# Optimization experiments

Hardware: AMD Instinct MI355X
Metric: run time of the kernel (lower is better)

Reference implementation:

```python
import jax, jax.numpy as jnp
import numpy as np

B, D, NF, L, G = 8192, 4096, 16, 32, 64  # batch, input_dim, num_factors, latent_per_factor, num groups
K = D // G  # group size (contiguous equal-size partition of columns)


def setup_inputs() -> dict:
    key = jax.random.key(0)
    k0, k1, k2, k3 = jax.random.split(key, 4)
    x = jax.random.normal(k0, (B, D), dtype=jnp.float32)
    # encoder: Linear(D,128) -> ReLU -> Linear(128, NF*L)
    W1 = jax.random.normal(k1, (D, 128), dtype=jnp.float32) * 0.02
    b1 = jnp.zeros((128,), dtype=jnp.float32)
    W2 = jax.random.normal(k2, (128, NF * L), dtype=jnp.float32) * 0.02
    b2 = jnp.zeros((NF * L,), dtype=jnp.float32)
    # k_matrix decoders: one [K, L] matrix per group, stacked -> [G, K, L]
    decoders = jax.random.normal(k3, (G, K, L), dtype=jnp.float32)
    return {"x": x, "W1": W1, "b1": b1, "W2": W2, "b2": b2, "decoders": decoders}


def reference(x, W1, b1, W2, b2, decoders):
    # encoder
    z = jax.nn.relu(x @ W1 + b1) @ W2 + b2                 # [B, NF*L]
    # reconstructions[:, group_g] = sum_j z_j @ D_g^T  ==  (sum_j z_j) @ D_g^T
    z_sum = z.reshape(x.shape[0], NF, L).sum(axis=1)        # [B, L]
    recon = jnp.einsum('bl,gkl->bgk', z_sum, decoders)      # [B, G, K]
    recon = recon.reshape(x.shape[0], G * K)                # [B, D] (contiguous groups)
    return (z, recon)
```

## Files before the change

kernel.cpp:

```cpp
#include <hip/hip_runtime.h>
#include <hip/hip_bf16.h>

#define BATCH 8192
#define DIN   4096
#define H1    128
#define NLAT  512
#define LAT   32
#define BM    32
#define BK    128
#define NSTEP (DIN / BK)
#define APITCH 136

typedef short bf16x8 __attribute__((ext_vector_type(8)));
typedef float f32x4  __attribute__((ext_vector_type(4)));

static __device__ __forceinline__ unsigned short f2bf(float f) {
  union { float f; unsigned u; } v; v.f = f;
  return (unsigned short)((v.u + 0x7FFFu + ((v.u >> 16) & 1u)) >> 16);
}

__global__ void prep_all(const float* __restrict__ W1, const float* __restrict__ W2,
                         const float* __restrict__ dec,
                         unsigned short* __restrict__ W1B,
                         unsigned short* __restrict__ W2B,
                         float* __restrict__ decT) {
  int b = blockIdx.x;
  int t = threadIdx.x;
  if (b < 256) {
    int gi = (b << 2) + (t >> 6);
    int lane = t & 63;
    int kb = ((gi >> 3) << 5) + ((lane >> 4) << 3);
    int c = ((gi & 7) << 4) + (lane & 15);
    union { bf16x8 v; unsigned short u[8]; } o;
#pragma unroll
    for (int j = 0; j < 8; j++) o.u[j] = f2bf(W1[(size_t)(kb + j) * H1 + c]);
    *(bf16x8*)(W1B + (((size_t)gi << 6) + lane) * 8) = o.v;
  } else if (b < 288) {
    int gi = ((b - 256) << 2) + (t >> 6);
    int lane = t & 63;
    int kb = ((gi >> 5) << 5) + ((lane >> 4) << 3);
    int c = ((gi & 31) << 4) + (lane & 15);
    union { bf16x8 v; unsigned short u[8]; } o;
#pragma unroll
    for (int j = 0; j < 8; j++) o.u[j] = f2bf(W2[(size_t)(kb + j) * NLAT + c]);
    *(bf16x8*)(W2B + (((size_t)gi << 6) + lane) * 8) = o.v;
  } else {
    __shared__ float tbuf[32][33];
    int d0 = (b - 288) * 32;
    int tx = t & 31, ty = t >> 5;
#pragma unroll
    for (int i = 0; i < 32; i += 8)
      tbuf[ty + i][tx] = dec[(size_t)(d0 + ty + i) * LAT + tx];
    __syncthreads();
#pragma unroll
    for (int i = 0; i < 32; i += 8)
      decT[(size_t)(ty + i) * DIN + (d0 + tx)] = tbuf[tx][ty + i];
  }
}

__global__ __launch_bounds__(512, 2) void enc_kernel(
    const float* __restrict__ x, const unsigned short* __restrict__ W1B,
    const unsigned short* __restrict__ W2B,
    const float* __restrict__ b1, const float* __restrict__ b2,
    float* __restrict__ zout, float* __restrict__ zsumg) {
  __shared__ unsigned short As[2][BM * APITCH];
  __shared__ unsigned short hs[BM * APITCH];
  __shared__ float zsp[8][32][32];

  const int t = threadIdx.x;
  const int rbase = blockIdx.x << 5;
  const int w = t >> 6, lane = t & 63;
  const int g = lane >> 4, fr = lane & 15;

  const int srow = t >> 4, skq = (t & 15) << 3;
  const float* xp = x + (size_t)(rbase + srow) * DIN + skq;
  const int wofs = srow * APITCH + skq;

  f32x4 acc[2];
  acc[0] = (f32x4){0.f, 0.f, 0.f, 0.f};
  acc[1] = (f32x4){0.f, 0.f, 0.f, 0.f};

  {
    f32x4 ra0 = *(const f32x4*)xp;
    f32x4 ra1 = *(const f32x4*)(xp + 4);
    union { bf16x8 v; unsigned short u[8]; } o;
#pragma unroll
    for (int j = 0; j < 4; j++) { o.u[j] = f2bf(ra0[j]); o.u[4 + j] = f2bf(ra1[j]); }
    *(bf16x8*)(&As[0][wofs]) = o.v;
  }
  __syncthreads();

  for (int s = 0; s < NSTEP; ++s) {
    f32x4 ra0, ra1;
    const bool more = (s + 1) < NSTEP;
    if (more) {
      ra0 = *(const f32x4*)(xp + (s + 1) * BK);
      ra1 = *(const f32x4*)(xp + (s + 1) * BK + 4);
    }
    const unsigned short* ab = &As[s & 1][0];
#pragma unroll
    for (int k32 = 0; k32 < 4; ++k32) {
      bf16x8 bv = *(const bf16x8*)(W1B + (((size_t)(((s << 2) + k32) << 3) + w) << 9) + (lane << 3));
      bf16x8 a0 = *(const bf16x8*)(ab + fr * APITCH + (((k32 << 2) + g) << 3));
      bf16x8 a1 = *(const bf16x8*)(ab + (16 + fr) * APITCH + (((k32 << 2) + g) << 3));
      acc[0] = __builtin_amdgcn_mfma_f32_16x16x32_bf16(a0, bv, acc[0], 0, 0, 0);
      acc[1] = __builtin_amdgcn_mfma_f32_16x16x32_bf16(a1, bv, acc[1], 0, 0, 0);
    }
    if (more) {
      union { bf16x8 v; unsigned short u[8]; } o;
#pragma unroll
      for (int j = 0; j < 4; j++) { o.u[j] = f2bf(ra0[j]); o.u[4 + j] = f2bf(ra1[j]); }
      *(bf16x8*)(&As[(s + 1) & 1][wofs]) = o.v;
    }
    __syncthreads();
  }

  {
    const int col = (w << 4) + fr;
    const float b1v = b1[col];
#pragma unroll
    for (int rg = 0; rg < 2; rg++)
#pragma unroll
      for (int j = 0; j < 4; j++) {
        float h = fmaxf(acc[rg][j] + b1v, 0.f);
        hs[((rg << 4) + (g << 2) + j) * APITCH + col] = f2bf(h);
      }
  }
  __syncthreads();

  f32x4 acc2[2][4];
#pragma unroll
  for (int i = 0; i < 2; i++)
#pragma unroll
    for (int j = 0; j < 4; j++) acc2[i][j] = (f32x4){0.f, 0.f, 0.f, 0.f};
#pragma unroll
  for (int k32 = 0; k32 < 4; ++k32) {
    bf16x8 a0 = *(const bf16x8*)(hs + fr * APITCH + (((k32 << 2) + g) << 3));
    bf16x8 a1 = *(const bf16x8*)(hs + (16 + fr) * APITCH + (((k32 << 2) + g) << 3));
#pragma unroll
    for (int cfl = 0; cfl < 4; ++cfl) {
      bf16x8 bv = *(const bf16x8*)(W2B + (((size_t)((k32 << 5) + (w << 2) + cfl)) << 9) + (lane << 3));
      acc2[0][cfl] = __builtin_amdgcn_mfma_f32_16x16x32_bf16(a0, bv, acc2[0][cfl], 0, 0, 0);
      acc2[1][cfl] = __builtin_amdgcn_mfma_f32_16x16x32_bf16(a1, bv, acc2[1][cfl], 0, 0, 0);
    }
  }

  {
    float b2v[4];
#pragma unroll
    for (int cfl = 0; cfl < 4; ++cfl) b2v[cfl] = b2[(w << 6) + (cfl << 4) + fr];
#pragma unroll
    for (int rg = 0; rg < 2; rg++) {
      f32x4 zv[4];
#pragma unroll
      for (int cfl = 0; cfl < 4; ++cfl) {
#pragma unroll
        for (int j = 0; j < 4; j++) zv[cfl][j] = acc2[rg][cfl][j] + b2v[cfl];
        const int row = rbase + (rg << 4) + (g << 2);
        const int col = (w << 6) + (cfl << 4) + fr;
#pragma unroll
        for (int j = 0; j < 4; j++)
          zout[(size_t)(row + j) * NLAT + col] = zv[cfl][j];
      }
#pragma unroll
      for (int j = 0; j < 4; j++) {
        const int row = (rg << 4) + (g << 2) + j;
        zsp[w][row][fr]      = zv[0][j] + zv[2][j];
        zsp[w][row][16 + fr] = zv[1][j] + zv[3][j];
      }
    }
  }
  __syncthreads();
#pragma unroll
  for (int i = 0; i < 2; i++) {
    int idx = t + (i << 9);
    int r = idx >> 5, l = idx & 31;
    float s = 0.f;
#pragma unroll
    for (int w8 = 0; w8 < 8; w8++) s += zsp[w8][r][l];
    zsumg[(size_t)(rbase + r) * LAT + l] = s;
  }
}

__global__ __launch_bounds__(256) void recon_kernel(
    const float* __restrict__ zsumg, const float* __restrict__ decT,
    float* __restrict__ rout) {
  __shared__ float zs[32][32];
  int t = threadIdx.x;
  int rbase = (blockIdx.x >> 4) << 5;
  int dcol0 = (blockIdx.x & 15) << 8;
  {
    int r = t >> 3, c4 = (t & 7) << 2;
    *(f32x4*)&zs[r][c4] = *(const f32x4*)(zsumg + (size_t)(rbase + r) * LAT + c4);
  }
  __syncthreads();
  int wq = t >> 6, lane = t & 63;
  int r0 = wq << 3;
  int dcol = dcol0 + (lane << 2);
  f32x4 acc[8];
#pragma unroll
  for (int r = 0; r < 8; r++) acc[r] = (f32x4){0.f, 0.f, 0.f, 0.f};
#pragma unroll 8
  for (int l = 0; l < 32; l++) {
    f32x4 dv = *(const f32x4*)(decT + (size_t)l * DIN + dcol);
#pragma unroll
    for (int r = 0; r < 8; r++) {
      float zv = zs[r0 + r][l];
#pragma unroll
      for (int j = 0; j < 4; j++) acc[r][j] += zv * dv[j];
    }
  }
#pragma unroll
  for (int r = 0; r < 8; r++)
    *(f32x4*)(rout + (size_t)(rbase + r0 + r) * DIN + dcol) = acc[r];
}

extern "C" void kernel_launch(void* const* d_in, const int* in_sizes, int n_in,
                              void* d_out, int out_size, void* d_ws, size_t ws_size,
                              hipStream_t stream) {
  const float* x   = (const float*)d_in[0];
  const float* W1  = (const float*)d_in[1];
  const float* b1  = (const float*)d_in[2];
  const float* W2  = (const float*)d_in[3];
  const float* b2  = (const float*)d_in[4];
  const float* dec = (const float*)d_in[5];
  float* zout = (float*)d_out;
  float* rout = zout + (size_t)BATCH * NLAT;

  char* ws = (char*)d_ws;
  unsigned short* W1B = (unsigned short*)ws;
  unsigned short* W2B = (unsigned short*)(ws + (1u << 20));
  float* decT  = (float*)(ws + (1u << 20) + (1u << 17));
  float* zsumg = (float*)(ws + (1u << 20) + (1u << 17) + (1u << 19));

  prep_all<<<dim3(416), 256, 0, stream>>>(W1, W2, dec, W1B, W2B, decT);
  enc_kernel<<<dim3(BATCH / BM), 512, 0, stream>>>(x, W1B, W2B, b1, b2, zout, zsumg);
  recon_kernel<<<dim3(4096), 256, 0, stream>>>(zsumg, decT, rout);
}
```

Measured before the change: 91.06 us.

## Fuse reconstruction into encoder kernel with smaller row tiles and deeper prefetch

Merges the encoder and reconstruction kernels into a single kernel. Each block now computes z for 16 rows, reduces z_sum in shared memory, then writes the 16x4096 reconstruction directly, which removes the zsumg round trip and one launch. The row tile drops from 32 to 16 so there are twice as many blocks, and x loads are prefetched four steps ahead. In exchange, W1 B-fragments are reused across half as many rows, and each block's tail now streams a large output with only 16 accumulators per thread, which may lengthen per-block time and add register pressure.

```diff
diff --git a/kernel.cpp b/kernel.cpp
--- a/kernel.cpp
+++ b/kernel.cpp
@@ -6,17 +6,25 @@
 #define H1    128
 #define NLAT  512
 #define LAT   32
-#define BM    32
+#define BM    16
 #define BK    128
 #define NSTEP (DIN / BK)
 #define APITCH 136
 
 typedef short bf16x8 __attribute__((ext_vector_type(8)));
+typedef short bf16x4 __attribute__((ext_vector_type(4)));
 typedef float f32x4  __attribute__((ext_vector_type(4)));
 
 static __device__ __forceinline__ unsigned short f2bf(float f) {
   union { float f; unsigned u; } v; v.f = f;
   return (unsigned short)((v.u + 0x7FFFu + ((v.u >> 16) & 1u)) >> 16);
+}
+
+static __device__ __forceinline__ void cvtw4(unsigned short* p, f32x4 v) {
+  union { bf16x4 v; unsigned short u[4]; } o;
+#pragma unroll
+  for (int j = 0; j < 4; j++) o.u[j] = f2bf(v[j]);
+  *(bf16x4*)p = o.v;
 }
 
 __global__ void prep_all(const float* __restrict__ W1, const float* __restrict__ W2,
@@ -58,161 +66,132 @@
   }
 }
 
-__global__ __launch_bounds__(512, 2) void enc_kernel(
+__global__ __launch_bounds__(512, 2) void fused_kernel(
     const float* __restrict__ x, const unsigned short* __restrict__ W1B,
     const unsigned short* __restrict__ W2B,
     const float* __restrict__ b1, const float* __restrict__ b2,
-    float* __restrict__ zout, float* __restrict__ zsumg) {
+    const float* __restrict__ decT,
+    float* __restrict__ zout, float* __restrict__ rout) {
   __shared__ unsigned short As[2][BM * APITCH];
   __shared__ unsigned short hs[BM * APITCH];
-  __shared__ float zsp[8][32][32];
+  __shared__ float zsp[8][BM][32];
+  __shared__ float zs[BM][32];
 
   const int t = threadIdx.x;
-  const int rbase = blockIdx.x << 5;
+  const int rbase = blockIdx.x << 4;
   const int w = t >> 6, lane = t & 63;
   const int g = lane >> 4, fr = lane & 15;
 
-  const int srow = t >> 4, skq = (t & 15) << 3;
+  const int srow = t >> 5, skq = (t & 31) << 2;
   const float* xp = x + (size_t)(rbase + srow) * DIN + skq;
   const int wofs = srow * APITCH + skq;
 
-  f32x4 acc[2];
-  acc[0] = (f32x4){0.f, 0.f, 0.f, 0.f};
-  acc[1] = (f32x4){0.f, 0.f, 0.f, 0.f};
-
-  {
-    f32x4 ra0 = *(const f32x4*)xp;
-    f32x4 ra1 = *(const f32x4*)(xp + 4);
-    union { bf16x8 v; unsigned short u[8]; } o;
-#pragma unroll
-    for (int j = 0; j < 4; j++) { o.u[j] = f2bf(ra0[j]); o.u[4 + j] = f2bf(ra1[j]); }
-    *(bf16x8*)(&As[0][wofs]) = o.v;
-  }
-  __syncthreads();
-
-  for (int s = 0; s < NSTEP; ++s) {
-    f32x4 ra0, ra1;
-    const bool more = (s + 1) < NSTEP;
-    if (more) {
-      ra0 = *(const f32x4*)(xp + (s + 1) * BK);
-      ra1 = *(const f32x4*)(xp + (s + 1) * BK + 4);
-    }
-    const unsigned short* ab = &As[s & 1][0];
-#pragma unroll
-    for (int k32 = 0; k32 < 4; ++k32) {
-      bf16x8 bv = *(const bf16x8*)(W1B + (((size_t)(((s << 2) + k32) << 3) + w) << 9) + (lane << 3));
-      bf16x8 a0 = *(const bf16x8*)(ab + fr * APITCH + (((k32 << 2) + g) << 3));
-      bf16x8 a1 = *(const bf16x8*)(ab + (16 + fr) * APITCH + (((k32 << 2) + g) << 3));
-      acc[0] = __builtin_amdgcn_mfma_f32_16x16x32_bf16(a0, bv, acc[0], 0, 0, 0);
-      acc[1] = __builtin_amdgcn_mfma_f32_16x16x32_bf16(a1, bv, acc[1], 0, 0, 0);
-    }
-    if (more) {
-      union { bf16x8 v; unsigned short u[8]; } o;
-#pragma unroll
-      for (int j = 0; j < 4; j++) { o.u[j] = f2bf(ra0[j]); o.u[4 + j] = f2bf(ra1[j]); }
-      *(bf16x8*)(&As[(s + 1) & 1][wofs]) = o.v;
-    }
-    __syncthreads();
-  }
+  f32x4 acc = (f32x4){0.f, 0.f, 0.f, 0.f};
+
+  cvtw4(&As[0][wofs], *(const f32x4*)xp);
+  f32x4 pf1 = *(const f32x4*)(xp + 1 * BK);
+  f32x4 pf2 = *(const f32x4*)(xp + 2 * BK);
+  f32x4 pf3 = *(const f32x4*)(xp + 3 * BK);
+  f32x4 pf0 = *(const f32x4*)(xp + 4 * BK);
+  __syncthreads();
+
+#define ASTEP(S, PF) do {                                                    \
+    const unsigned short* ab = &As[(S) & 1][0];                              \
+    _Pragma("unroll")                                                        \
+    for (int k32 = 0; k32 < 4; ++k32) {                                      \
+      bf16x8 bv = *(const bf16x8*)(W1B +                                     \
+          ((((size_t)(((S) << 2) + k32) << 3) + w) << 9) + (lane << 3));     \
+      bf16x8 a0 = *(const bf16x8*)(ab + fr * APITCH + (((k32 << 2) + g) << 3)); \
+      acc = __builtin_amdgcn_mfma_f32_16x16x32_bf16(a0, bv, acc, 0, 0, 0);   \
+    }                                                                        \
+    if ((S) + 1 < NSTEP) {                                                   \
+      cvtw4(&As[((S) + 1) & 1][wofs], PF);                                   \
+      if ((S) + 5 < NSTEP) PF = *(const f32x4*)(xp + ((S) + 5) * BK);        \
+    }                                                                        \
+    __syncthreads();                                                         \
+  } while (0)
+
+  for (int s = 0; s < NSTEP; s += 4) {
+    ASTEP(s, pf1);
+    ASTEP(s + 1, pf2);
+    ASTEP(s + 2, pf3);
+    ASTEP(s + 3, pf0);
+  }
+#undef ASTEP
 
   {
     const int col = (w << 4) + fr;
     const float b1v = b1[col];
 #pragma unroll
-    for (int rg = 0; rg < 2; rg++)
-#pragma unroll
-      for (int j = 0; j < 4; j++) {
-        float h = fmaxf(acc[rg][j] + b1v, 0.f);
-        hs[((rg << 4) + (g << 2) + j) * APITCH + col] = f2bf(h);
-      }
-  }
-  __syncthreads();
-
-  f32x4 acc2[2][4];
-#pragma unroll
-  for (int i = 0; i < 2; i++)
-#pragma unroll
-    for (int j = 0; j < 4; j++) acc2[i][j] = (f32x4){0.f, 0.f, 0.f, 0.f};
+    for (int j = 0; j < 4; j++) {
+      float h = fmaxf(acc[j] + b1v, 0.f);
+      hs[((g << 2) + j) * APITCH + col] = f2bf(h);
+    }
+  }
+  __syncthreads();
+
+  f32x4 acc2[4];
+#pragma unroll
+  for (int i = 0; i < 4; i++) acc2[i] = (f32x4){0.f, 0.f, 0.f, 0.f};
 #pragma unroll
   for (int k32 = 0; k32 < 4; ++k32) {
     bf16x8 a0 = *(const bf16x8*)(hs + fr * APITCH + (((k32 << 2) + g) << 3));
-    bf16x8 a1 = *(const bf16x8*)(hs + (16 + fr) * APITCH + (((k32 << 2) + g) << 3));
 #pragma unroll
     for (int cfl = 0; cfl < 4; ++cfl) {
-      bf16x8 bv = *(const bf16x8*)(W2B + (((size_t)((k32 << 5) + (w << 2) + cfl)) << 9) + (lane << 3));
-      acc2[0][cfl] = __builtin_amdgcn_mfma_f32_16x16x32_bf16(a0, bv, acc2[0][cfl], 0, 0, 0);
-      acc2[1][cfl] = __builtin_amdgcn_mfma_f32_16x16x32_bf16(a1, bv, acc2[1][cfl], 0, 0, 0);
-    }
-  }
-
+      bf16x8 bv = *(const bf16x8*)(W2B +
+          (((size_t)((k32 << 5) + (w << 2) + cfl)) << 9) + (lane << 3));
+      acc2[cfl] = __builtin_amdgcn_mfma_f32_16x16x32_bf16(a0, bv, acc2[cfl], 0, 0, 0);
+    }
+  }
   {
-    float b2v[4];
-#pragma unroll
-    for (int cfl = 0; cfl < 4; ++cfl) b2v[cfl] = b2[(w << 6) + (cfl << 4) + fr];
-#pragma unroll
-    for (int rg = 0; rg < 2; rg++) {
-      f32x4 zv[4];
-#pragma unroll
-      for (int cfl = 0; cfl < 4; ++cfl) {
-#pragma unroll
-        for (int j = 0; j < 4; j++) zv[cfl][j] = acc2[rg][cfl][j] + b2v[cfl];
-        const int row = rbase + (rg << 4) + (g << 2);
-        const int col = (w << 6) + (cfl << 4) + fr;
-#pragma unroll
-        for (int j = 0; j < 4; j++)
-          zout[(size_t)(row + j) * NLAT + col] = zv[cfl][j];
+    f32x4 zv[4];
+#pragma unroll
+    for (int cfl = 0; cfl < 4; ++cfl) {
+      const float b2v = b2[(w << 6) + (cfl << 4) + fr];
+#pragma unroll
+      for (int j = 0; j < 4; j++) zv[cfl][j] = acc2[cfl][j] + b2v;
+    }
+    const int row0 = g << 2;
+#pragma unroll
+    for (int j = 0; j < 4; j++) {
+#pragma unroll
+      for (int cfl = 0; cfl < 4; ++cfl)
+        zout[(size_t)(rbase + row0 + j) * NLAT + (w << 6) + (cfl << 4) + fr] = zv[cfl][j];
+      zsp[w][row0 + j][fr]      = zv[0][j] + zv[2][j];
+      zsp[w][row0 + j][16 + fr] = zv[1][j] + zv[3][j];
+    }
+  }
+  __syncthreads();
+  {
+    const int r = t >> 5, l = t & 31;
+    float s = 0.f;
+#pragma unroll
+    for (int w8 = 0; w8 < 8; w8++) s += zsp[w8][r][l];
+    zs[r][l] = s;
+  }
+  __syncthreads();
+
+  const int dbase = (w << 9) + (lane << 2);
+#pragma unroll
+  for (int pass = 0; pass < 2; ++pass) {
+    const int dcol = dbase + (pass << 8);
+    f32x4 a[16];
+#pragma unroll
+    for (int r = 0; r < 16; ++r) a[r] = (f32x4){0.f, 0.f, 0.f, 0.f};
+#pragma unroll 4
+    for (int l = 0; l < 32; ++l) {
+      f32x4 dv = *(const f32x4*)(decT + (size_t)l * DIN + dcol);
+#pragma unroll
+      for (int r = 0; r < 16; ++r) {
+        const float zvv = zs[r][l];
+#pragma unroll
+        for (int j = 0; j < 4; j++) a[r][j] += zvv * dv[j];
       }
-#pragma unroll
-      for (int j = 0; j < 4; j++) {
-        const int row = (rg << 4) + (g << 2) + j;
-        zsp[w][row][fr]      = zv[0][j] + zv[2][j];
-        zsp[w][row][16 + fr] = zv[1][j] + zv[3][j];
-      }
-    }
-  }
-  __syncthreads();
-#pragma unroll
-  for (int i = 0; i < 2; i++) {
-    int idx = t + (i << 9);
-    int r = idx >> 5, l = idx & 31;
-    float s = 0.f;
-#pragma unroll
-    for (int w8 = 0; w8 < 8; w8++) s += zsp[w8][r][l];
-    zsumg[(size_t)(rbase + r) * LAT + l] = s;
-  }
-}
-
-__global__ __launch_bounds__(256) void recon_kernel(
-    const float* __restrict__ zsumg, const float* __restrict__ decT,
-    float* __restrict__ rout) {
-  __shared__ float zs[32][32];
-  int t = threadIdx.x;
-  int rbase = (blockIdx.x >> 4) << 5;
-  int dcol0 = (blockIdx.x & 15) << 8;
-  {
-    int r = t >> 3, c4 = (t & 7) << 2;
-    *(f32x4*)&zs[r][c4] = *(const f32x4*)(zsumg + (size_t)(rbase + r) * LAT + c4);
-  }
-  __syncthreads();
-  int wq = t >> 6, lane = t & 63;
-  int r0 = wq << 3;
-  int dcol = dcol0 + (lane << 2);
-  f32x4 acc[8];
-#pragma unroll
-  for (int r = 0; r < 8; r++) acc[r] = (f32x4){0.f, 0.f, 0.f, 0.f};
-#pragma unroll 8
-  for (int l = 0; l < 32; l++) {
-    f32x4 dv = *(const f32x4*)(decT + (size_t)l * DIN + dcol);
-#pragma unroll
-    for (int r = 0; r < 8; r++) {
-      float zv = zs[r0 + r][l];
-#pragma unroll
-      for (int j = 0; j < 4; j++) acc[r][j] += zv * dv[j];
-    }
-  }
-#pragma unroll
-  for (int r = 0; r < 8; r++)
-    *(f32x4*)(rout + (size_t)(rbase + r0 + r) * DIN + dcol) = acc[r];
+    }
+#pragma unroll
+    for (int r = 0; r < 16; ++r)
+      *(f32x4*)(rout + (size_t)(rbase + r) * DIN + dcol) = a[r];
+  }
 }
 
 extern "C" void kernel_launch(void* const* d_in, const int* in_sizes, int n_in,
@@ -230,10 +209,8 @@
   char* ws = (char*)d_ws;
   unsigned short* W1B = (unsigned short*)ws;
   unsigned short* W2B = (unsigned short*)(ws + (1u << 20));
-  float* decT  = (float*)(ws + (1u << 20) + (1u << 17));
-  float* zsumg = (float*)(ws + (1u << 20) + (1u << 17) + (1u << 19));
+  float* decT = (float*)(ws + (1u << 20) + (1u << 17));
 
   prep_all<<<dim3(416), 256, 0, stream>>>(W1, W2, dec, W1B, W2B, decT);
-  enc_kernel<<<dim3(BATCH / BM), 512, 0, stream>>>(x, W1B, W2B, b1, b2, zout, zsumg);
-  recon_kernel<<<dim3(4096), 256, 0, stream>>>(zsumg, decT, rout);
-}
+  fused_kernel<<<dim3(BATCH / BM), 512, 0, stream>>>(x, W1B, W2B, b1, b2, decT, zout, rout);
+}
```

After: 106.9 us. +17.4%, slower.

## Halve encoder row tile to 16 rows with 256-thread blocks and 4 waves

Applied to the files above, without the earlier changes.

The encoder kernel now handles 16 batch rows per block with 4 waves of 256 threads instead of 32 rows with 8 waves. Each wave computes two column tiles of the first layer and eight of the second. The grid doubles to 512 blocks and the launch bounds allow 4 blocks per CU, giving more parallelism across CUs. In exchange, every W1/W2 fragment loaded from global memory now feeds only one 16-row MFMA instead of two, roughly doubling weight traffic per row; the recon kernel unroll is also lowered from 8 to 4.

```diff
diff --git a/kernel.cpp b/kernel.cpp
--- a/kernel.cpp
+++ b/kernel.cpp
@@ -6,7 +6,7 @@
 #define H1    128
 #define NLAT  512
 #define LAT   32
-#define BM    32
+#define BM    16
 #define BK    128
 #define NSTEP (DIN / BK)
 #define APITCH 136
@@ -17,6 +17,13 @@
 static __device__ __forceinline__ unsigned short f2bf(float f) {
   union { float f; unsigned u; } v; v.f = f;
   return (unsigned short)((v.u + 0x7FFFu + ((v.u >> 16) & 1u)) >> 16);
+}
+
+static __device__ __forceinline__ void cvtw8(unsigned short* p, f32x4 a, f32x4 b) {
+  union { bf16x8 v; unsigned short u[8]; } o;
+#pragma unroll
+  for (int j = 0; j < 4; j++) { o.u[j] = f2bf(a[j]); o.u[4 + j] = f2bf(b[j]); }
+  *(bf16x8*)p = o.v;
 }
 
 __global__ void prep_all(const float* __restrict__ W1, const float* __restrict__ W2,
@@ -34,7 +41,7 @@
     union { bf16x8 v; unsigned short u[8]; } o;
 #pragma unroll
     for (int j = 0; j < 8; j++) o.u[j] = f2bf(W1[(size_t)(kb + j) * H1 + c]);
-    *(bf16x8*)(W1B + (((size_t)gi << 6) + lane) * 8) = o.v;
+    *(bf16x8*)(W1B + (((size_t)gi << 6) + (lane & 63)) * 8) = o.v;
   } else if (b < 288) {
     int gi = ((b - 256) << 2) + (t >> 6);
     int lane = t & 63;
@@ -58,17 +65,17 @@
   }
 }
 
-__global__ __launch_bounds__(512, 2) void enc_kernel(
+__global__ __launch_bounds__(256, 4) void enc_kernel(
     const float* __restrict__ x, const unsigned short* __restrict__ W1B,
     const unsigned short* __restrict__ W2B,
     const float* __restrict__ b1, const float* __restrict__ b2,
     float* __restrict__ zout, float* __restrict__ zsumg) {
   __shared__ unsigned short As[2][BM * APITCH];
   __shared__ unsigned short hs[BM * APITCH];
-  __shared__ float zsp[8][32][32];
+  __shared__ float zsp[4][BM][33];
 
   const int t = threadIdx.x;
-  const int rbase = blockIdx.x << 5;
+  const int rbase = blockIdx.x << 4;
   const int w = t >> 6, lane = t & 63;
   const int g = lane >> 4, fr = lane & 15;
 
@@ -80,14 +87,7 @@
   acc[0] = (f32x4){0.f, 0.f, 0.f, 0.f};
   acc[1] = (f32x4){0.f, 0.f, 0.f, 0.f};
 
-  {
-    f32x4 ra0 = *(const f32x4*)xp;
-    f32x4 ra1 = *(const f32x4*)(xp + 4);
-    union { bf16x8 v; unsigned short u[8]; } o;
-#pragma unroll
-    for (int j = 0; j < 4; j++) { o.u[j] = f2bf(ra0[j]); o.u[4 + j] = f2bf(ra1[j]); }
-    *(bf16x8*)(&As[0][wofs]) = o.v;
-  }
+  cvtw8(&As[0][wofs], *(const f32x4*)xp, *(const f32x4*)(xp + 4));
   __syncthreads();
 
   for (int s = 0; s < NSTEP; ++s) {
@@ -100,84 +100,71 @@
     const unsigned short* ab = &As[s & 1][0];
 #pragma unroll
     for (int k32 = 0; k32 < 4; ++k32) {
-      bf16x8 bv = *(const bf16x8*)(W1B + (((size_t)(((s << 2) + k32) << 3) + w) << 9) + (lane << 3));
       bf16x8 a0 = *(const bf16x8*)(ab + fr * APITCH + (((k32 << 2) + g) << 3));
-      bf16x8 a1 = *(const bf16x8*)(ab + (16 + fr) * APITCH + (((k32 << 2) + g) << 3));
-      acc[0] = __builtin_amdgcn_mfma_f32_16x16x32_bf16(a0, bv, acc[0], 0, 0, 0);
-      acc[1] = __builtin_amdgcn_mfma_f32_16x16x32_bf16(a1, bv, acc[1], 0, 0, 0);
-    }
-    if (more) {
-      union { bf16x8 v; unsigned short u[8]; } o;
-#pragma unroll
-      for (int j = 0; j < 4; j++) { o.u[j] = f2bf(ra0[j]); o.u[4 + j] = f2bf(ra1[j]); }
-      *(bf16x8*)(&As[(s + 1) & 1][wofs]) = o.v;
-    }
+#pragma unroll
+      for (int cc = 0; cc < 2; ++cc) {
+        bf16x8 bv = *(const bf16x8*)(W1B +
+            ((((size_t)(((s << 2) + k32) << 3)) + (w << 1) + cc) << 9) + (lane << 3));
+        acc[cc] = __builtin_amdgcn_mfma_f32_16x16x32_bf16(a0, bv, acc[cc], 0, 0, 0);
+      }
+    }
+    if (more)
+      cvtw8(&As[(s + 1) & 1][wofs], ra0, ra1);
     __syncthreads();
   }
 
   {
-    const int col = (w << 4) + fr;
-    const float b1v = b1[col];
-#pragma unroll
-    for (int rg = 0; rg < 2; rg++)
+#pragma unroll
+    for (int cc = 0; cc < 2; ++cc) {
+      const int col = (w << 5) + (cc << 4) + fr;
+      const float b1v = b1[col];
 #pragma unroll
       for (int j = 0; j < 4; j++) {
-        float h = fmaxf(acc[rg][j] + b1v, 0.f);
-        hs[((rg << 4) + (g << 2) + j) * APITCH + col] = f2bf(h);
+        float h = fmaxf(acc[cc][j] + b1v, 0.f);
+        hs[((g << 2) + j) * APITCH + col] = f2bf(h);
       }
-  }
-  __syncthreads();
-
-  f32x4 acc2[2][4];
-#pragma unroll
-  for (int i = 0; i < 2; i++)
-#pragma unroll
-    for (int j = 0; j < 4; j++) acc2[i][j] = (f32x4){0.f, 0.f, 0.f, 0.f};
+    }
+  }
+  __syncthreads();
+
+  f32x4 acc2[8];
+#pragma unroll
+  for (int i = 0; i < 8; i++) acc2[i] = (f32x4){0.f, 0.f, 0.f, 0.f};
 #pragma unroll
   for (int k32 = 0; k32 < 4; ++k32) {
     bf16x8 a0 = *(const bf16x8*)(hs + fr * APITCH + (((k32 << 2) + g) << 3));
-    bf16x8 a1 = *(const bf16x8*)(hs + (16 + fr) * APITCH + (((k32 << 2) + g) << 3));
-#pragma unroll
-    for (int cfl = 0; cfl < 4; ++cfl) {
-      bf16x8 bv = *(const bf16x8*)(W2B + (((size_t)((k32 << 5) + (w << 2) + cfl)) << 9) + (lane << 3));
-      acc2[0][cfl] = __builtin_amdgcn_mfma_f32_16x16x32_bf16(a0, bv, acc2[0][cfl], 0, 0, 0);
-      acc2[1][cfl] = __builtin_amdgcn_mfma_f32_16x16x32_bf16(a1, bv, acc2[1][cfl], 0, 0, 0);
+#pragma unroll
+    for (int cc = 0; cc < 8; ++cc) {
+      bf16x8 bv = *(const bf16x8*)(W2B +
+          (((size_t)((k32 << 5) + (w << 3) + cc)) << 9) + (lane << 3));
+      acc2[cc] = __builtin_amdgcn_mfma_f32_16x16x32_bf16(a0, bv, acc2[cc], 0, 0, 0);
     }
   }
 
   {
-    float b2v[4];
-#pragma unroll
-    for (int cfl = 0; cfl < 4; ++cfl) b2v[cfl] = b2[(w << 6) + (cfl << 4) + fr];
-#pragma unroll
-    for (int rg = 0; rg < 2; rg++) {
-      f32x4 zv[4];
-#pragma unroll
-      for (int cfl = 0; cfl < 4; ++cfl) {
-#pragma unroll
-        for (int j = 0; j < 4; j++) zv[cfl][j] = acc2[rg][cfl][j] + b2v[cfl];
-        const int row = rbase + (rg << 4) + (g << 2);
-        const int col = (w << 6) + (cfl << 4) + fr;
-#pragma unroll
-        for (int j = 0; j < 4; j++)
-          zout[(size_t)(row + j) * NLAT + col] = zv[cfl][j];
-      }
-#pragma unroll
-      for (int j = 0; j < 4; j++) {
-        const int row = (rg << 4) + (g << 2) + j;
-        zsp[w][row][fr]      = zv[0][j] + zv[2][j];
-        zsp[w][row][16 + fr] = zv[1][j] + zv[3][j];
-      }
+    f32x4 zv[8];
+#pragma unroll
+    for (int cc = 0; cc < 8; ++cc) {
+      const float b2v = b2[(w << 7) + (cc << 4) + fr];
+#pragma unroll
+      for (int j = 0; j < 4; j++) zv[cc][j] = acc2[cc][j] + b2v;
+    }
+    const int row0 = g << 2;
+#pragma unroll
+    for (int j = 0; j < 4; j++) {
+#pragma unroll
+      for (int cc = 0; cc < 8; ++cc)
+        zout[(size_t)(rbase + row0 + j) * NLAT + (w << 7) + (cc << 4) + fr] = zv[cc][j];
+      zsp[w][row0 + j][fr]      = zv[0][j] + zv[2][j] + zv[4][j] + zv[6][j];
+      zsp[w][row0 + j][16 + fr] = zv[1][j] + zv[3][j] + zv[5][j] + zv[7][j];
     }
   }
   __syncthreads();
 #pragma unroll
   for (int i = 0; i < 2; i++) {
-    int idx = t + (i << 9);
+    int idx = t + (i << 8);
     int r = idx >> 5, l = idx & 31;
-    float s = 0.f;
-#pragma unroll
-    for (int w8 = 0; w8 < 8; w8++) s += zsp[w8][r][l];
+    float s = zsp[0][r][l] + zsp[1][r][l] + zsp[2][r][l] + zsp[3][r][l];
     zsumg[(size_t)(rbase + r) * LAT + l] = s;
   }
 }
@@ -200,7 +187,7 @@
   f32x4 acc[8];
 #pragma unroll
   for (int r = 0; r < 8; r++) acc[r] = (f32x4){0.f, 0.f, 0.f, 0.f};
-#pragma unroll 8
+#pragma unroll 4
   for (int l = 0; l < 32; l++) {
     f32x4 dv = *(const f32x4*)(decT + (size_t)l * DIN + dcol);
 #pragma unroll
@@ -234,6 +221,6 @@
   float* zsumg = (float*)(ws + (1u << 20) + (1u << 17) + (1u << 19));
 
   prep_all<<<dim3(416), 256, 0, stream>>>(W1, W2, dec, W1B, W2B, decT);
-  enc_kernel<<<dim3(BATCH / BM), 512, 0, stream>>>(x, W1B, W2B, b1, b2, zout, zsumg);
+  enc_kernel<<<dim3(BATCH / BM), 256, 0, stream>>>(x, W1B, W2B, b1, b2, zout, zsumg);
   recon_kernel<<<dim3(4096), 256, 0, stream>>>(zsumg, decT, rout);
 }
```

New measurement: 90.93 us. Within noise of the previous version (-0.1%).
